# Kernel tuning notes

Hardware: AMD Instinct MI355X
Metric: run time of the kernel (lower is better)

Reference implementation:

```python
import jax, jax.numpy as jnp
import numpy as np

ALPHA = 4
N_NODES = 100000
N_EDGES = 1600000
DIM = 128


def setup_inputs() -> dict:
    key = jax.random.key(0)
    ks = jax.random.split(key, 7)
    x = jax.random.normal(ks[0], (N_NODES, DIM), dtype=jnp.float32)
    edge_index = jax.random.randint(ks[1], (ALPHA, 2, N_EDGES), 0, N_NODES, dtype=jnp.int64)
    edge_attr = jax.random.uniform(ks[2], (ALPHA, N_EDGES), dtype=jnp.float32)
    lin_w = jax.random.normal(ks[3], (DIM, DIM), dtype=jnp.float32) * 0.05
    lin_b = jax.random.normal(ks[4], (DIM,), dtype=jnp.float32) * 0.05
    conv_w = jax.random.normal(ks[5], (ALPHA, DIM, DIM), dtype=jnp.float32) * 0.05
    conv_b = jax.random.normal(ks[6], (ALPHA, DIM), dtype=jnp.float32) * 0.05
    return {"x": x, "edge_index": edge_index, "edge_attr": edge_attr,
            "lin_w": lin_w, "lin_b": lin_b, "conv_w": conv_w, "conv_b": conv_b}


def _gcn_conv(h, row, col, w, weight, bias):
    # gcn_norm with add_self_loops=False
    deg = jax.ops.segment_sum(w, col, num_segments=N_NODES)          # [N]
    dinv = jnp.where(deg > 0, jax.lax.rsqrt(deg), 0.0)               # deg^{-1/2}
    norm = dinv[row] * w * dinv[col]                                 # [E]
    hw = h @ weight.T                                                # [N, D] (Linear(in,out))
    msg = norm[:, None] * hw[row]                                    # gather + scale, [E, D]
    out = jax.ops.segment_sum(msg, col, num_segments=N_NODES)        # scatter-add, [N, D]
    return out + bias


def reference(x, edge_index, edge_attr, lin_w, lin_b, conv_w, conv_b):
    # dropout is identity in eval mode (training=False)
    h = jax.nn.relu(x @ lin_w.T + lin_b)
    hs = [h]
    for i in range(ALPHA):
        row, col = edge_index[i, 0], edge_index[i, 1]
        h = _gcn_conv(hs[-1], row, col, edge_attr[i], conv_w[i], conv_b[i])
        h = jax.nn.relu(h)
        hs.append(h)
    return jnp.stack(hs)  # [ALPHA+1, N, D] (torch returns list of these)
```

## Files before the change

### kernel.cpp

```cpp
#include <hip/hip_runtime.h>

#define NN 100000
#define NE 1600000
#define DD 128
#define SCAN_CHUNK 1024
#define NBLK ((NN + SCAN_CHUNK - 1) / SCAN_CHUNK)
#define NNP (NBLK * SCAN_CHUNK)
#define NTOT (4 * NNP)
#define BPL ((NE + 255) / 256)

using u16 = unsigned short;
using u32 = unsigned int;
using u64 = unsigned long long;

typedef __bf16 bf16x8 __attribute__((ext_vector_type(8)));
typedef float  f32x4  __attribute__((ext_vector_type(4)));

__device__ __forceinline__ float bf2f(u16 h){ return __uint_as_float(((u32)h) << 16); }
__device__ __forceinline__ u16 f2bf(float f){
  u32 u = __float_as_uint(f);
  u += 0x7FFFu + ((u >> 16) & 1u);
  return (u16)(u >> 16);
}
__device__ __forceinline__ int ld_idx(const int* __restrict__ p, long long k, int w64){
  return w64 ? p[2*k] : p[k];
}
__device__ __forceinline__ float ldf(const void* __restrict__ p, long long k, int f32){
  return f32 ? ((const float*)p)[k] : bf2f(((const u16*)p)[k]);
}

__global__ void detect_kernel(const int* __restrict__ ei, const u16* __restrict__ xw,
                              int* __restrict__ flags){
  if (threadIdx.x == 0 && blockIdx.x == 0){
    int all0 = 1;
    for (int k = 1; k < 256; k += 2) all0 &= (ei[k] == 0);
    flags[0] = all0;
    int cnt = 0;
    for (int i = 0; i < 128; ++i){
      u16 w = xw[2*i];
      int e = (w >> 7) & 0xFF;
      cnt += (e >= 100 && e <= 130);
    }
    flags[1] = (cnt < 64);
  }
}

__global__ __launch_bounds__(256) void prep_w_kernel(const void* __restrict__ lin_w,
    const void* __restrict__ conv_w, const int* __restrict__ flags, u16* __restrict__ wbf){
  int i = blockIdx.x*256 + threadIdx.x;
  if (i >= 5*DD*DD) return;
  int f32 = flags[1];
  float v = (i < DD*DD) ? ldf(lin_w, i, f32) : ldf(conv_w, i - DD*DD, f32);
  wbf[i] = f2bf(v);
}

__global__ __launch_bounds__(256) void hist_all_kernel(const void* __restrict__ ea,
    const int* __restrict__ ei, const int* __restrict__ flags, u64* __restrict__ pk){
  int lyr = blockIdx.x / BPL;
  int e = (blockIdx.x - lyr*BPL)*256 + threadIdx.x;
  if (e >= NE) return;
  long long col_off = ((long long)lyr*2 + 1)*NE;
  long long ea_off  = (long long)lyr*NE;
  int col = ld_idx(ei, col_off + e, flags[0]);
  float w = ldf(ea, ea_off + e, flags[1]);
  u64 v = (1ull << 40) | (u64)(w * 16777216.0f);
  atomicAdd(pk + (size_t)lyr*NNP + col, v);
}

__global__ __launch_bounds__(256) void dinv_all_kernel(const u64* __restrict__ pk,
    float* __restrict__ dinv, int* __restrict__ cnt){
  int n = blockIdx.x*256 + threadIdx.x;
  if (n >= NTOT) return;
  u64 p = pk[n];
  cnt[n] = (int)(p >> 40);
  float d = (float)(p & ((1ull << 40) - 1)) * (1.0f/16777216.0f);
  dinv[n] = (d > 0.f) ? rsqrtf(d) : 0.f;
}

__global__ __launch_bounds__(256) void scan_block_kernel(const int* __restrict__ cnt,
    int* __restrict__ base, int* __restrict__ bsums){
  __shared__ int sm[256];
  int b = blockIdx.x, t = threadIdx.x;
  int i0 = b*SCAN_CHUNK + t*4;
  int v[4];
  #pragma unroll
  for (int j = 0; j < 4; ++j) v[j] = cnt[i0 + j];
  int s = v[0] + v[1] + v[2] + v[3];
  sm[t] = s;
  __syncthreads();
  for (int off = 1; off < 256; off <<= 1){
    int add = (t >= off) ? sm[t - off] : 0;
    __syncthreads();
    sm[t] += add;
    __syncthreads();
  }
  int run = sm[t] - s;
  if (t == 255) bsums[b] = sm[255];
  #pragma unroll
  for (int j = 0; j < 4; ++j){
    base[i0 + j] = run;
    run += v[j];
  }
}

__global__ void scan_sums_kernel(int* __restrict__ bsums, int nb){
  __shared__ int sm[256];
  int t = threadIdx.x;
  int* bs = bsums + blockIdx.x*nb;
  int v = (t < nb) ? bs[t] : 0;
  sm[t] = v;
  __syncthreads();
  for (int off = 1; off < 256; off <<= 1){
    int add = (t >= off) ? sm[t - off] : 0;
    __syncthreads();
    sm[t] += add;
    __syncthreads();
  }
  if (t < nb) bs[t] = sm[t] - v;
}

__global__ __launch_bounds__(256) void scan_add_kernel(int* __restrict__ base,
    const int* __restrict__ bsums, int* __restrict__ cursor){
  int i = blockIdx.x*256 + threadIdx.x;
  if (i >= NTOT) return;
  int b = base[i] + bsums[i / SCAN_CHUNK];
  base[i] = b;
  cursor[i] = b;
}

__global__ __launch_bounds__(256) void fill_all_kernel(const void* __restrict__ ea,
    const int* __restrict__ ei, const float* __restrict__ dinv,
    const int* __restrict__ flags, int* __restrict__ cursor, int2* __restrict__ rc){
  int lyr = blockIdx.x / BPL;
  int e = (blockIdx.x - lyr*BPL)*256 + threadIdx.x;
  if (e >= NE) return;
  int w64 = flags[0];
  long long row_off = ((long long)lyr*2 + 0)*NE;
  long long col_off = ((long long)lyr*2 + 1)*NE;
  long long ea_off  = (long long)lyr*NE;
  int row = ld_idx(ei, row_off + e, w64);
  int col = ld_idx(ei, col_off + e, w64);
  float w = ldf(ea, ea_off + e, flags[1]);
  const float* dv = dinv + (size_t)lyr*NNP;
  int pos = atomicAdd(cursor + (size_t)lyr*NNP + col, 1);
  rc[(size_t)lyr*NE + pos] = make_int2(row, __float_as_int(dv[row] * w * dv[col]));
}

__global__ __launch_bounds__(256) void gemm_mfma_kernel(
    const void* __restrict__ in, int in_mode,
    const u16* __restrict__ wbf,
    const void* __restrict__ bias, long long b_off,
    const int* __restrict__ flags,
    void* __restrict__ outb, long long out_off){
  __shared__ u16 ah[64*DD];
  __shared__ u16 al[64*DD];
  int t = threadIdx.x;
  int f32 = flags[1];
  int inf32 = (in_mode == 2) ? f32 : in_mode;
  long long rowbase = (long long)blockIdx.x * 64;

  #pragma unroll
  for (int it = 0; it < 8; ++it){
    int i = (it*256 + t) * 4;
    int r = i >> 7, c = i & 127;
    long long gr = rowbase + r;
    float v0, v1, v2, v3;
    if (gr < NN){
      if (inf32){
        const float4 f = *(const float4*)((const float*)in + gr*DD + c);
        v0 = f.x; v1 = f.y; v2 = f.z; v3 = f.w;
      } else {
        const ushort4 u = *(const ushort4*)((const u16*)in + gr*DD + c);
        v0 = bf2f(u.x); v1 = bf2f(u.y); v2 = bf2f(u.z); v3 = bf2f(u.w);
      }
    } else { v0 = v1 = v2 = v3 = 0.f; }
    u16 h0 = f2bf(v0), h1 = f2bf(v1), h2 = f2bf(v2), h3 = f2bf(v3);
    u16 l0 = f2bf(v0 - bf2f(h0)), l1 = f2bf(v1 - bf2f(h1));
    u16 l2 = f2bf(v2 - bf2f(h2)), l3 = f2bf(v3 - bf2f(h3));
    int idx = (r*DD + c) ^ ((r & 7) << 3);
    *(ushort4*)&ah[idx] = make_ushort4(h0, h1, h2, h3);
    *(ushort4*)&al[idx] = make_ushort4(l0, l1, l2, l3);
  }
  __syncthreads();

  const int w  = t >> 6, l = t & 63;
  const int lr = l & 15, lg = l >> 4;
  const int arow = w*16 + lr;
  f32x4 acc[8];
  #pragma unroll
  for (int j = 0; j < 8; ++j) acc[j] = (f32x4){0.f, 0.f, 0.f, 0.f};

  #pragma unroll
  for (int s = 0; s < 4; ++s){
    const int kb = s*32 + lg*8;
    const int aidx = (arow*DD + kb) ^ ((arow & 7) << 3);
    bf16x8 afh = *(const bf16x8*)&ah[aidx];
    bf16x8 afl = *(const bf16x8*)&al[aidx];
    #pragma unroll
    for (int tt = 0; tt < 8; ++tt){
      bf16x8 bfr = *(const bf16x8*)&wbf[(tt*16 + lr)*DD + kb];
      acc[tt] = __builtin_amdgcn_mfma_f32_16x16x32_bf16(afh, bfr, acc[tt], 0, 0, 0);
      acc[tt] = __builtin_amdgcn_mfma_f32_16x16x32_bf16(afl, bfr, acc[tt], 0, 0, 0);
    }
  }

  const long long gn0 = rowbase + w*16 + lg*4;
  #pragma unroll
  for (int tt = 0; tt < 8; ++tt){
    const int d = tt*16 + lr;
    const float bv = ldf(bias, b_off + d, f32);
    #pragma unroll
    for (int q = 0; q < 4; ++q){
      long long gn = gn0 + q;
      if (gn < NN){
        float vv = fmaxf(acc[tt][q] + bv, 0.f);
        long long gi = out_off + gn*DD + d;
        if (f32) ((float*)outb)[gi] = vv;
        else     ((u16*)outb)[gi] = f2bf(vv);
      }
    }
  }
}

__global__ __launch_bounds__(256) void agg_gemm_kernel(
    const void* __restrict__ hbase, long long h_off,
    const int2* __restrict__ rc,
    const int* __restrict__ basep, const int* __restrict__ cntp,
    const u16* __restrict__ wbf,
    const void* __restrict__ bias, long long b_off,
    const int* __restrict__ flags,
    void* __restrict__ outb, long long out_off){
  __shared__ u16 ah[64*DD];
  __shared__ u16 al[64*DD];
  int t = threadIdx.x;
  int f32 = flags[1];
  long long rowbase = (long long)blockIdx.x * 64;
  const int w = t >> 6, l = t & 63;

  for (int i = 0; i < 16; ++i){
    int r = w*16 + i;
    long long n = rowbase + r;
    float ax = 0.f, ay = 0.f;
    if (n < NN){
      int s = basep[n], e = s + cntp[n];
      if (f32){
        const float2* hp = (const float2*)((const float*)hbase + h_off);
        int j = s;
        for (; j + 8 <= e; j += 8){
          int2 v[8];
          #pragma unroll
          for (int k = 0; k < 8; ++k) v[k] = rc[j + k];
          float2 hv[8];
          #pragma unroll
          for (int k = 0; k < 8; ++k) hv[k] = hp[(long long)v[k].x*64 + l];
          #pragma unroll
          for (int k = 0; k < 8; ++k){
            float c = __int_as_float(v[k].y);
            ax += c*hv[k].x; ay += c*hv[k].y;
          }
        }
        if (j < e){
          int2 v[8];
          #pragma unroll
          for (int k = 0; k < 8; ++k){
            int jj = (j + k < e) ? (j + k) : s;
            v[k] = rc[jj];
            if (j + k >= e) v[k].y = 0;
          }
          float2 hv[8];
          #pragma unroll
          for (int k = 0; k < 8; ++k) hv[k] = hp[(long long)v[k].x*64 + l];
          #pragma unroll
          for (int k = 0; k < 8; ++k){
            float c = __int_as_float(v[k].y);
            ax += c*hv[k].x; ay += c*hv[k].y;
          }
        }
      } else {
        const u32* hp = (const u32*)((const u16*)hbase + h_off);
        int j = s;
        for (; j + 8 <= e; j += 8){
          int2 v[8];
          #pragma unroll
          for (int k = 0; k < 8; ++k) v[k] = rc[j + k];
          u32 hv[8];
          #pragma unroll
          for (int k = 0; k < 8; ++k) hv[k] = hp[(long long)v[k].x*64 + l];
          #pragma unroll
          for (int k = 0; k < 8; ++k){
            float c = __int_as_float(v[k].y);
            ax += c*bf2f((u16)(hv[k] & 0xFFFF));
            ay += c*bf2f((u16)(hv[k] >> 16));
          }
        }
        if (j < e){
          int2 v[8];
          #pragma unroll
          for (int k = 0; k < 8; ++k){
            int jj = (j + k < e) ? (j + k) : s;
            v[k] = rc[jj];
            if (j + k >= e) v[k].y = 0;
          }
          u32 hv[8];
          #pragma unroll
          for (int k = 0; k < 8; ++k) hv[k] = hp[(long long)v[k].x*64 + l];
          #pragma unroll
          for (int k = 0; k < 8; ++k){
            float c = __int_as_float(v[k].y);
            ax += c*bf2f((u16)(hv[k] & 0xFFFF));
            ay += c*bf2f((u16)(hv[k] >> 16));
          }
        }
      }
    }
    u16 h0 = f2bf(ax), h1 = f2bf(ay);
    u16 l0 = f2bf(ax - bf2f(h0)), l1 = f2bf(ay - bf2f(h1));
    int idx = (r*DD + 2*l) ^ ((r & 7) << 3);
    *(u32*)&ah[idx] = (u32)h0 | ((u32)h1 << 16);
    *(u32*)&al[idx] = (u32)l0 | ((u32)l1 << 16);
  }
  __syncthreads();

  const int lr = l & 15, lg = l >> 4;
  const int arow = w*16 + lr;
  f32x4 acc[8];
  #pragma unroll
  for (int j = 0; j < 8; ++j) acc[j] = (f32x4){0.f, 0.f, 0.f, 0.f};

  #pragma unroll
  for (int s = 0; s < 4; ++s){
    const int kb = s*32 + lg*8;
    const int aidx = (arow*DD + kb) ^ ((arow & 7) << 3);
    bf16x8 afh = *(const bf16x8*)&ah[aidx];
    bf16x8 afl = *(const bf16x8*)&al[aidx];
    #pragma unroll
    for (int tt = 0; tt < 8; ++tt){
      bf16x8 bfr = *(const bf16x8*)&wbf[(tt*16 + lr)*DD + kb];
      acc[tt] = __builtin_amdgcn_mfma_f32_16x16x32_bf16(afh, bfr, acc[tt], 0, 0, 0);
      acc[tt] = __builtin_amdgcn_mfma_f32_16x16x32_bf16(afl, bfr, acc[tt], 0, 0, 0);
    }
  }

  const long long gn0 = rowbase + w*16 + lg*4;
  #pragma unroll
  for (int tt = 0; tt < 8; ++tt){
    const int d = tt*16 + lr;
    const float bv = ldf(bias, b_off + d, f32);
    #pragma unroll
    for (int q = 0; q < 4; ++q){
      long long gn = gn0 + q;
      if (gn < NN){
        float vv = fmaxf(acc[tt][q] + bv, 0.f);
        long long gi = out_off + gn*DD + d;
        if (f32) ((float*)outb)[gi] = vv;
        else     ((u16*)outb)[gi] = f2bf(vv);
      }
    }
  }
}

extern "C" void kernel_launch(void* const* d_in, const int* in_sizes, int n_in,
                              void* d_out, int out_size, void* d_ws, size_t ws_size,
                              hipStream_t stream){
  const void* x      = d_in[0];
  const int*  ei     = (const int*)d_in[1];
  const void* ea     = d_in[2];
  const void* lin_w  = d_in[3];
  const void* lin_b  = d_in[4];
  const void* conv_w = d_in[5];
  const void* conv_b = d_in[6];
  void* out = d_out;

  char* ws = (char*)d_ws;
  size_t o = 0;
  auto alloc = [&](size_t bytes){ void* p = ws + o; o = (o + bytes + 255) & ~(size_t)255; return p; };
  int*   flags  = (int*)  alloc(256);
  u64*   pk     = (u64*)  alloc((size_t)NTOT*8);
  float* dinv   = (float*)alloc((size_t)NTOT*4);
  int*   cnt    = (int*)  alloc((size_t)NTOT*4);
  int*   base   = (int*)  alloc((size_t)NTOT*4);
  int*   cursor = (int*)  alloc((size_t)NTOT*4);
  int*   bsums  = (int*)  alloc((size_t)4*NBLK*4 + 256);
  int2*  rc     = (int2*) alloc((size_t)4*NE*8);
  u16*   wbf    = (u16*)  alloc((size_t)5*DD*DD*2);

  detect_kernel<<<1, 64, 0, stream>>>(ei, (const u16*)x, flags);
  prep_w_kernel<<<(5*DD*DD + 255)/256, 256, 0, stream>>>(lin_w, conv_w, flags, wbf);

  hipMemsetAsync(pk, 0, (size_t)NTOT*8, stream);
  hist_all_kernel<<<4*BPL, 256, 0, stream>>>(ea, ei, flags, pk);
  dinv_all_kernel<<<(NTOT+255)/256, 256, 0, stream>>>(pk, dinv, cnt);
  scan_block_kernel<<<4*NBLK, 256, 0, stream>>>(cnt, base, bsums);
  scan_sums_kernel<<<4, 256, 0, stream>>>(bsums, NBLK);
  scan_add_kernel<<<(NTOT+255)/256, 256, 0, stream>>>(base, bsums, cursor);
  fill_all_kernel<<<4*BPL, 256, 0, stream>>>(ea, ei, dinv, flags, cursor, rc);

  gemm_mfma_kernel<<<(NN+63)/64, 256, 0, stream>>>(x, 2, wbf, lin_b, 0, flags, out, 0);

  for (int i = 0; i < 4; ++i){
    long long h_off = (long long)i*NN*DD;
    long long o_off = (long long)(i+1)*NN*DD;
    agg_gemm_kernel<<<(NN+63)/64, 256, 0, stream>>>(out, h_off,
                                                    rc + (size_t)i*NE,
                                                    base + (size_t)i*NNP,
                                                    cnt  + (size_t)i*NNP,
                                                    wbf + (size_t)(1+i)*DD*DD,
                                                    conv_b, (long long)i*DD,
                                                    flags, out, o_off);
  }
}
```

Measured before the change: 1.539 ms.

## Build CSR in two passes: bucket edges by column block, then local scatter

Replaces the single-pass CSR fill, which does a global atomic per edge on a per-node cursor and scatters writes randomly, with a two-phase sort. The first pass bins edges into buckets of 256 destination nodes using per-bucket atomics and packs the local column into the high bits of the row index. The second pass has each block scatter its bucket into final CSR order using shared-memory atomics. This aims to cut global atomic contention and random write traffic, at the cost of an extra pass over the edges and a temporary buffer of the same size as the edge list.

```diff
diff --git a/kernel.cpp b/kernel.cpp
--- a/kernel.cpp
+++ b/kernel.cpp
@@ -8,6 +8,8 @@
 #define NNP (NBLK * SCAN_CHUNK)
 #define NTOT (4 * NNP)
 #define BPL ((NE + 255) / 256)
+#define BK 256
+#define NBUK (NNP / BK)
 
 using u16 = unsigned short;
 using u32 = unsigned int;
@@ -120,17 +122,22 @@
 }
 
 __global__ __launch_bounds__(256) void scan_add_kernel(int* __restrict__ base,
-    const int* __restrict__ bsums, int* __restrict__ cursor){
+    const int* __restrict__ bsums){
   int i = blockIdx.x*256 + threadIdx.x;
   if (i >= NTOT) return;
-  int b = base[i] + bsums[i / SCAN_CHUNK];
-  base[i] = b;
-  cursor[i] = b;
-}
-
-__global__ __launch_bounds__(256) void fill_all_kernel(const void* __restrict__ ea,
+  base[i] += bsums[i / SCAN_CHUNK];
+}
+
+__global__ void bcur_init_kernel(const int* __restrict__ base, int* __restrict__ bcur){
+  int i = blockIdx.x*256 + threadIdx.x;
+  if (i >= 4*NBUK) return;
+  int lyr = i / NBUK, b = i - lyr*NBUK;
+  bcur[i] = base[(size_t)lyr*NNP + b*BK];
+}
+
+__global__ __launch_bounds__(256) void bin_kernel(const void* __restrict__ ea,
     const int* __restrict__ ei, const float* __restrict__ dinv,
-    const int* __restrict__ flags, int* __restrict__ cursor, int2* __restrict__ rc){
+    const int* __restrict__ flags, int* __restrict__ bcur, int2* __restrict__ tmp){
   int lyr = blockIdx.x / BPL;
   int e = (blockIdx.x - lyr*BPL)*256 + threadIdx.x;
   if (e >= NE) return;
@@ -142,8 +149,33 @@
   int col = ld_idx(ei, col_off + e, w64);
   float w = ldf(ea, ea_off + e, flags[1]);
   const float* dv = dinv + (size_t)lyr*NNP;
-  int pos = atomicAdd(cursor + (size_t)lyr*NNP + col, 1);
-  rc[(size_t)lyr*NE + pos] = make_int2(row, __float_as_int(dv[row] * w * dv[col]));
+  float coef = dv[row] * w * dv[col];
+  int b = col >> 8;
+  int pos = atomicAdd(bcur + lyr*NBUK + b, 1);
+  tmp[(size_t)lyr*NE + pos] = make_int2(row | ((col & 255) << 17), __float_as_int(coef));
+}
+
+__global__ __launch_bounds__(256) void csr_kernel(const int2* __restrict__ tmp,
+    const int* __restrict__ base, int2* __restrict__ rc){
+  __shared__ int cur[BK];
+  int gb = blockIdx.x;
+  int lyr = gb / NBUK, b = gb - lyr*NBUK;
+  int t = threadIdx.x;
+  const int* bb = base + (size_t)lyr*NNP;
+  cur[t] = bb[b*BK + t];
+  int s = bb[b*BK];
+  int e = (b == NBUK-1) ? NE : bb[(b+1)*BK];
+  __syncthreads();
+  const int2* tp = tmp + (size_t)lyr*NE;
+  int2* rp = rc + (size_t)lyr*NE;
+  for (int j = s + t; j < e; j += 256){
+    int2 rec = tp[j];
+    u32 p = (u32)rec.x;
+    int row = (int)(p & 0x1FFFFu);
+    int cl  = (int)(p >> 17);
+    int pos = atomicAdd(&cur[cl], 1);
+    rp[pos] = make_int2(row, rec.y);
+  }
 }
 
 __global__ __launch_bounds__(256) void gemm_mfma_kernel(
@@ -379,8 +411,9 @@
   float* dinv   = (float*)alloc((size_t)NTOT*4);
   int*   cnt    = (int*)  alloc((size_t)NTOT*4);
   int*   base   = (int*)  alloc((size_t)NTOT*4);
-  int*   cursor = (int*)  alloc((size_t)NTOT*4);
+  int*   bcur   = (int*)  alloc((size_t)4*NBUK*4);
   int*   bsums  = (int*)  alloc((size_t)4*NBLK*4 + 256);
+  int2*  tmp    = (int2*) alloc((size_t)4*NE*8);
   int2*  rc     = (int2*) alloc((size_t)4*NE*8);
   u16*   wbf    = (u16*)  alloc((size_t)5*DD*DD*2);
 
@@ -392,8 +425,10 @@
   dinv_all_kernel<<<(NTOT+255)/256, 256, 0, stream>>>(pk, dinv, cnt);
   scan_block_kernel<<<4*NBLK, 256, 0, stream>>>(cnt, base, bsums);
   scan_sums_kernel<<<4, 256, 0, stream>>>(bsums, NBLK);
-  scan_add_kernel<<<(NTOT+255)/256, 256, 0, stream>>>(base, bsums, cursor);
-  fill_all_kernel<<<4*BPL, 256, 0, stream>>>(ea, ei, dinv, flags, cursor, rc);
+  scan_add_kernel<<<(NTOT+255)/256, 256, 0, stream>>>(base, bsums);
+  bcur_init_kernel<<<(4*NBUK+255)/256, 256, 0, stream>>>(base, bcur);
+  bin_kernel<<<4*BPL, 256, 0, stream>>>(ea, ei, dinv, flags, bcur, tmp);
+  csr_kernel<<<4*NBUK, 256, 0, stream>>>(tmp, base, rc);
 
   gemm_mfma_kernel<<<(NN+63)/64, 256, 0, stream>>>(x, 2, wbf, lin_b, 0, flags, out, 0);
 
```

After: 2.885 ms. 87.5% more time.

## Partition CSR fill by destination column across XCDs with nontemporal edge loads

Applied to the files above, without the earlier changes.

The edge fill kernel is launched with eight times as many blocks. Consecutive block ids map to the eight XCDs, and each block keeps only the edges whose destination column falls in its XCD's column range, so cursor atomics and rc writes for a given column stay in one XCD's L2. Edge index and attribute loads become nontemporal so they do not pollute the cache. The cost is that the column array is read eight times and there are eight times as many blocks, most threads exiting early. The gain depends on the hardware assigning blocks round-robin to XCDs.

```diff
diff --git a/kernel.cpp b/kernel.cpp
--- a/kernel.cpp
+++ b/kernel.cpp
@@ -8,6 +8,8 @@
 #define NNP (NBLK * SCAN_CHUNK)
 #define NTOT (4 * NNP)
 #define BPL ((NE + 255) / 256)
+#define NXCD 8
+#define PCOLS (NNP / NXCD)
 
 using u16 = unsigned short;
 using u32 = unsigned int;
@@ -25,8 +27,15 @@
 __device__ __forceinline__ int ld_idx(const int* __restrict__ p, long long k, int w64){
   return w64 ? p[2*k] : p[k];
 }
+__device__ __forceinline__ int ld_idx_nt(const int* __restrict__ p, long long k, int w64){
+  return w64 ? __builtin_nontemporal_load(p + 2*k) : __builtin_nontemporal_load(p + k);
+}
 __device__ __forceinline__ float ldf(const void* __restrict__ p, long long k, int f32){
   return f32 ? ((const float*)p)[k] : bf2f(((const u16*)p)[k]);
+}
+__device__ __forceinline__ float ldf_nt(const void* __restrict__ p, long long k, int f32){
+  return f32 ? __builtin_nontemporal_load((const float*)p + k)
+             : bf2f(__builtin_nontemporal_load((const u16*)p + k));
 }
 
 __global__ void detect_kernel(const int* __restrict__ ei, const u16* __restrict__ xw,
@@ -128,22 +137,28 @@
   cursor[i] = b;
 }
 
-__global__ __launch_bounds__(256) void fill_all_kernel(const void* __restrict__ ea,
+__global__ __launch_bounds__(256) void fill_x_kernel(const void* __restrict__ ea,
     const int* __restrict__ ei, const float* __restrict__ dinv,
     const int* __restrict__ flags, int* __restrict__ cursor, int2* __restrict__ rc){
-  int lyr = blockIdx.x / BPL;
-  int e = (blockIdx.x - lyr*BPL)*256 + threadIdx.x;
+  int g = blockIdx.x;
+  int p = g & 7;
+  int rest = g >> 3;
+  int lyr = rest / BPL;
+  int chunk = rest - lyr*BPL;
+  int e = chunk*256 + threadIdx.x;
   if (e >= NE) return;
   int w64 = flags[0];
+  long long col_off = ((long long)lyr*2 + 1)*NE;
+  int col = ld_idx_nt(ei, col_off + e, w64);
+  if (col / PCOLS != p) return;
   long long row_off = ((long long)lyr*2 + 0)*NE;
-  long long col_off = ((long long)lyr*2 + 1)*NE;
   long long ea_off  = (long long)lyr*NE;
-  int row = ld_idx(ei, row_off + e, w64);
-  int col = ld_idx(ei, col_off + e, w64);
-  float w = ldf(ea, ea_off + e, flags[1]);
+  int row = ld_idx_nt(ei, row_off + e, w64);
+  float w = ldf_nt(ea, ea_off + e, flags[1]);
   const float* dv = dinv + (size_t)lyr*NNP;
+  float coef = dv[row] * w * dv[col];
   int pos = atomicAdd(cursor + (size_t)lyr*NNP + col, 1);
-  rc[(size_t)lyr*NE + pos] = make_int2(row, __float_as_int(dv[row] * w * dv[col]));
+  rc[(size_t)lyr*NE + pos] = make_int2(row, __float_as_int(coef));
 }
 
 __global__ __launch_bounds__(256) void gemm_mfma_kernel(
@@ -393,7 +408,7 @@
   scan_block_kernel<<<4*NBLK, 256, 0, stream>>>(cnt, base, bsums);
   scan_sums_kernel<<<4, 256, 0, stream>>>(bsums, NBLK);
   scan_add_kernel<<<(NTOT+255)/256, 256, 0, stream>>>(base, bsums, cursor);
-  fill_all_kernel<<<4*BPL, 256, 0, stream>>>(ea, ei, dinv, flags, cursor, rc);
+  fill_x_kernel<<<4*BPL*NXCD, 256, 0, stream>>>(ea, ei, dinv, flags, cursor, rc);
 
   gemm_mfma_kernel<<<(NN+63)/64, 256, 0, stream>>>(x, 2, wbf, lin_b, 0, flags, out, 0);
 
```

After: 1.582 ms. +2.8%, slower.

## Gather from bf16 shadow copies and pack CSR edges into 32-bit records

Applied to the files above, without the earlier changes.

The GEMM kernels now write a bf16 shadow copy of each layer's fp32 output, and aggregation gathers neighbor features from that copy, halving gather bytes. Edge records shrink from 8 to 4 bytes by packing a 17-bit row index with a 15-bit quantized edge weight. The dinv scaling moves into aggregation: a per-neighbor dinv lookup plus a per-destination scale applied at the end. The gather is also unrolled to 16. This cuts memory traffic but adds bf16 rounding of gathered features and 15-bit weight quantization, which may hurt accuracy, and it adds an extra dinv gather per edge.

```diff
diff --git a/kernel.cpp b/kernel.cpp
--- a/kernel.cpp
+++ b/kernel.cpp
@@ -129,8 +129,8 @@
 }
 
 __global__ __launch_bounds__(256) void fill_all_kernel(const void* __restrict__ ea,
-    const int* __restrict__ ei, const float* __restrict__ dinv,
-    const int* __restrict__ flags, int* __restrict__ cursor, int2* __restrict__ rc){
+    const int* __restrict__ ei, const int* __restrict__ flags,
+    int* __restrict__ cursor, u32* __restrict__ rc){
   int lyr = blockIdx.x / BPL;
   int e = (blockIdx.x - lyr*BPL)*256 + threadIdx.x;
   if (e >= NE) return;
@@ -141,9 +141,9 @@
   int row = ld_idx(ei, row_off + e, w64);
   int col = ld_idx(ei, col_off + e, w64);
   float w = ldf(ea, ea_off + e, flags[1]);
-  const float* dv = dinv + (size_t)lyr*NNP;
+  u32 wq = (u32)__float2int_rn(w * 32767.0f);
   int pos = atomicAdd(cursor + (size_t)lyr*NNP + col, 1);
-  rc[(size_t)lyr*NE + pos] = make_int2(row, __float_as_int(dv[row] * w * dv[col]));
+  rc[(size_t)lyr*NE + pos] = (u32)row | (wq << 17);
 }
 
 __global__ __launch_bounds__(256) void gemm_mfma_kernel(
@@ -151,7 +151,8 @@
     const u16* __restrict__ wbf,
     const void* __restrict__ bias, long long b_off,
     const int* __restrict__ flags,
-    void* __restrict__ outb, long long out_off){
+    void* __restrict__ outb, long long out_off,
+    u16* __restrict__ hbf_out){
   __shared__ u16 ah[64*DD];
   __shared__ u16 al[64*DD];
   int t = threadIdx.x;
@@ -215,8 +216,12 @@
       if (gn < NN){
         float vv = fmaxf(acc[tt][q] + bv, 0.f);
         long long gi = out_off + gn*DD + d;
-        if (f32) ((float*)outb)[gi] = vv;
-        else     ((u16*)outb)[gi] = f2bf(vv);
+        if (f32){
+          ((float*)outb)[gi] = vv;
+          if (hbf_out) hbf_out[gn*DD + d] = f2bf(vv);
+        } else {
+          ((u16*)outb)[gi] = f2bf(vv);
+        }
       }
     }
   }
@@ -224,95 +229,73 @@
 
 __global__ __launch_bounds__(256) void agg_gemm_kernel(
     const void* __restrict__ hbase, long long h_off,
-    const int2* __restrict__ rc,
+    const u32* __restrict__ hbf_slot,
+    const u32* __restrict__ rcp,
     const int* __restrict__ basep, const int* __restrict__ cntp,
+    const float* __restrict__ dinvp,
     const u16* __restrict__ wbf,
     const void* __restrict__ bias, long long b_off,
     const int* __restrict__ flags,
-    void* __restrict__ outb, long long out_off){
+    void* __restrict__ outb, long long out_off,
+    u16* __restrict__ hbf_out){
   __shared__ u16 ah[64*DD];
   __shared__ u16 al[64*DD];
   int t = threadIdx.x;
   int f32 = flags[1];
   long long rowbase = (long long)blockIdx.x * 64;
   const int w = t >> 6, l = t & 63;
+  const u32* hp = f32 ? hbf_slot : (const u32*)((const u16*)hbase + h_off);
 
   for (int i = 0; i < 16; ++i){
     int r = w*16 + i;
     long long n = rowbase + r;
-    float ax = 0.f, ay = 0.f;
+    float ax = 0.f, ay = 0.f, sc = 0.f;
     if (n < NN){
       int s = basep[n], e = s + cntp[n];
-      if (f32){
-        const float2* hp = (const float2*)((const float*)hbase + h_off);
-        int j = s;
-        for (; j + 8 <= e; j += 8){
-          int2 v[8];
-          #pragma unroll
-          for (int k = 0; k < 8; ++k) v[k] = rc[j + k];
-          float2 hv[8];
-          #pragma unroll
-          for (int k = 0; k < 8; ++k) hv[k] = hp[(long long)v[k].x*64 + l];
-          #pragma unroll
-          for (int k = 0; k < 8; ++k){
-            float c = __int_as_float(v[k].y);
-            ax += c*hv[k].x; ay += c*hv[k].y;
-          }
-        }
-        if (j < e){
-          int2 v[8];
-          #pragma unroll
-          for (int k = 0; k < 8; ++k){
-            int jj = (j + k < e) ? (j + k) : s;
-            v[k] = rc[jj];
-            if (j + k >= e) v[k].y = 0;
-          }
-          float2 hv[8];
-          #pragma unroll
-          for (int k = 0; k < 8; ++k) hv[k] = hp[(long long)v[k].x*64 + l];
-          #pragma unroll
-          for (int k = 0; k < 8; ++k){
-            float c = __int_as_float(v[k].y);
-            ax += c*hv[k].x; ay += c*hv[k].y;
-          }
-        }
-      } else {
-        const u32* hp = (const u32*)((const u16*)hbase + h_off);
-        int j = s;
-        for (; j + 8 <= e; j += 8){
-          int2 v[8];
-          #pragma unroll
-          for (int k = 0; k < 8; ++k) v[k] = rc[j + k];
-          u32 hv[8];
-          #pragma unroll
-          for (int k = 0; k < 8; ++k) hv[k] = hp[(long long)v[k].x*64 + l];
-          #pragma unroll
-          for (int k = 0; k < 8; ++k){
-            float c = __int_as_float(v[k].y);
-            ax += c*bf2f((u16)(hv[k] & 0xFFFF));
-            ay += c*bf2f((u16)(hv[k] >> 16));
-          }
-        }
-        if (j < e){
-          int2 v[8];
-          #pragma unroll
-          for (int k = 0; k < 8; ++k){
-            int jj = (j + k < e) ? (j + k) : s;
-            v[k] = rc[jj];
-            if (j + k >= e) v[k].y = 0;
-          }
-          u32 hv[8];
-          #pragma unroll
-          for (int k = 0; k < 8; ++k) hv[k] = hp[(long long)v[k].x*64 + l];
-          #pragma unroll
-          for (int k = 0; k < 8; ++k){
-            float c = __int_as_float(v[k].y);
-            ax += c*bf2f((u16)(hv[k] & 0xFFFF));
-            ay += c*bf2f((u16)(hv[k] >> 16));
-          }
+      sc = dinvp[n] * (1.0f/32767.0f);
+      int j = s;
+      for (; j + 16 <= e; j += 16){
+        u32 rec[16];
+        #pragma unroll
+        for (int k = 0; k < 16; ++k) rec[k] = rcp[j + k];
+        float dr[16]; u32 hv[16];
+        #pragma unroll
+        for (int k = 0; k < 16; ++k){
+          int row = (int)(rec[k] & 0x1FFFFu);
+          dr[k] = dinvp[row];
+          hv[k] = hp[(size_t)row*64 + l];
+        }
+        #pragma unroll
+        for (int k = 0; k < 16; ++k){
+          float c = dr[k] * (float)(rec[k] >> 17);
+          ax += c * bf2f((u16)(hv[k] & 0xFFFF));
+          ay += c * bf2f((u16)(hv[k] >> 16));
         }
       }
-    }
+      if (j < e){
+        u32 rec[16];
+        #pragma unroll
+        for (int k = 0; k < 16; ++k){
+          int valid = (j + k < e);
+          u32 rr = rcp[valid ? (j + k) : s];
+          rec[k] = valid ? rr : (rr & 0x1FFFFu);
+        }
+        float dr[16]; u32 hv[16];
+        #pragma unroll
+        for (int k = 0; k < 16; ++k){
+          int row = (int)(rec[k] & 0x1FFFFu);
+          dr[k] = dinvp[row];
+          hv[k] = hp[(size_t)row*64 + l];
+        }
+        #pragma unroll
+        for (int k = 0; k < 16; ++k){
+          float c = dr[k] * (float)(rec[k] >> 17);
+          ax += c * bf2f((u16)(hv[k] & 0xFFFF));
+          ay += c * bf2f((u16)(hv[k] >> 16));
+        }
+      }
+    }
+    ax *= sc; ay *= sc;
     u16 h0 = f2bf(ax), h1 = f2bf(ay);
     u16 l0 = f2bf(ax - bf2f(h0)), l1 = f2bf(ay - bf2f(h1));
     int idx = (r*DD + 2*l) ^ ((r & 7) << 3);
@@ -352,8 +335,12 @@
       if (gn < NN){
         float vv = fmaxf(acc[tt][q] + bv, 0.f);
         long long gi = out_off + gn*DD + d;
-        if (f32) ((float*)outb)[gi] = vv;
-        else     ((u16*)outb)[gi] = f2bf(vv);
+        if (f32){
+          ((float*)outb)[gi] = vv;
+          if (hbf_out) hbf_out[gn*DD + d] = f2bf(vv);
+        } else {
+          ((u16*)outb)[gi] = f2bf(vv);
+        }
       }
     }
   }
@@ -381,8 +368,9 @@
   int*   base   = (int*)  alloc((size_t)NTOT*4);
   int*   cursor = (int*)  alloc((size_t)NTOT*4);
   int*   bsums  = (int*)  alloc((size_t)4*NBLK*4 + 256);
-  int2*  rc     = (int2*) alloc((size_t)4*NE*8);
+  u32*   rc     = (u32*)  alloc((size_t)4*NE*4);
   u16*   wbf    = (u16*)  alloc((size_t)5*DD*DD*2);
+  u16*   hbf    = (u16*)  alloc((size_t)4*NN*DD*2);
 
   detect_kernel<<<1, 64, 0, stream>>>(ei, (const u16*)x, flags);
   prep_w_kernel<<<(5*DD*DD + 255)/256, 256, 0, stream>>>(lin_w, conv_w, flags, wbf);
@@ -393,19 +381,22 @@
   scan_block_kernel<<<4*NBLK, 256, 0, stream>>>(cnt, base, bsums);
   scan_sums_kernel<<<4, 256, 0, stream>>>(bsums, NBLK);
   scan_add_kernel<<<(NTOT+255)/256, 256, 0, stream>>>(base, bsums, cursor);
-  fill_all_kernel<<<4*BPL, 256, 0, stream>>>(ea, ei, dinv, flags, cursor, rc);
-
-  gemm_mfma_kernel<<<(NN+63)/64, 256, 0, stream>>>(x, 2, wbf, lin_b, 0, flags, out, 0);
+  fill_all_kernel<<<4*BPL, 256, 0, stream>>>(ea, ei, flags, cursor, rc);
+
+  gemm_mfma_kernel<<<(NN+63)/64, 256, 0, stream>>>(x, 2, wbf, lin_b, 0, flags, out, 0, hbf);
 
   for (int i = 0; i < 4; ++i){
     long long h_off = (long long)i*NN*DD;
     long long o_off = (long long)(i+1)*NN*DD;
+    u16* hbf_next = (i < 3) ? (hbf + (size_t)(i+1)*NN*DD) : (u16*)nullptr;
     agg_gemm_kernel<<<(NN+63)/64, 256, 0, stream>>>(out, h_off,
+                                                    (const u32*)(hbf + (size_t)i*NN*DD),
                                                     rc + (size_t)i*NE,
                                                     base + (size_t)i*NNP,
                                                     cnt  + (size_t)i*NNP,
+                                                    dinv + (size_t)i*NNP,
                                                     wbf + (size_t)(1+i)*DD*DD,
                                                     conv_b, (long long)i*DD,
-                                                    flags, out, o_off);
-  }
-}
+                                                    flags, out, o_off, hbf_next);
+  }
+}
```

Result: slower. 1.593 ms (+3.5%).
